# Kernel tuning notes

Hardware: AMD Instinct MI355X
Metric: run time of the kernel (lower is better)

Reference implementation:

```python
import jax, jax.numpy as jnp
import numpy as np

D_K = 64


def setup_inputs() -> dict:
    key = jax.random.key(0)
    ks = jax.random.split(key, 12)
    b, n, t, k = 16, 2048, 12, 32
    d_q, d_k, d_c, n_head, d_out = 32, 64, 10, 4, 32
    return {
        "x": jax.random.normal(ks[0], (b, n, t, k), dtype=jnp.float32),
        "dis_mat": jax.random.uniform(ks[1], (n, n), dtype=jnp.float32),
        "K_S": jax.random.normal(ks[2], (n_head, d_k), dtype=jnp.float32) * 0.1,
        "V_S": jax.random.normal(ks[3], (n_head, n, d_c), dtype=jnp.float32) * 0.05,
        "K_T": jax.random.normal(ks[4], (n_head, d_k), dtype=jnp.float32) * 0.1,
        "V_T": jax.random.normal(ks[5], (n_head, n, d_c), dtype=jnp.float32) * 0.05,
        "W_Q0": jax.random.normal(ks[6], (k, d_q), dtype=jnp.float32) * 0.1,
        "W_QS": jax.random.normal(ks[7], (n * d_q, d_k), dtype=jnp.float32) * 0.01,
        "W_QT": jax.random.normal(ks[8], (t * d_q, d_k), dtype=jnp.float32) * 0.05,
        "W2": jax.random.normal(ks[9], (k, d_out), dtype=jnp.float32) * 0.1,
        "W_s0": jax.random.normal(ks[10], (k, d_out), dtype=jnp.float32) * 0.1,
        "W_s1": jax.random.normal(ks[11], (k, d_out), dtype=jnp.float32) * 0.1,
    }


def reference(x, dis_mat, K_S, V_S, K_T, V_T, W_Q0, W_QS, W_QT, W2, W_s0, W_s1):
    b, n, t, k = x.shape
    scale = 1.0 / jnp.sqrt(jnp.float32(D_K))
    # Q_0 projection: [b,n,t,d_q]
    out = x @ W_Q0
    # temporal / spatial queries -> [b, d_k]
    qt = out.mean(axis=1).reshape(b, -1) @ W_QT
    qs = out.mean(axis=2).reshape(b, -1) @ W_QS
    # head attention weights: [b, n_head]
    attn_t = jax.nn.softmax((qt * scale) @ K_T.T, axis=1)
    attn_s = jax.nn.softmax((qs * scale) @ K_S.T, axis=1)
    # head-mixed node embeddings: [b, n, d_c]
    et = jnp.einsum('hnc,bh->bnc', V_T, attn_t)
    es = jnp.einsum('hnc,bh->bnc', V_S, attn_s)
    ets = et + es
    # dynamic adjacency: [b, n, n]
    adj = jnp.einsum('bnc,bmc->bnm', ets, ets)
    adj = jax.nn.softmax(jax.nn.relu(dis_mat[None] + adj), axis=2)
    # graph conv chain over [b, t, n, d_out]
    xp = jnp.transpose(x, (0, 2, 1, 3))  # [b,t,n,k]
    z = xp @ W2
    for W in (W_s0, W_s1):
        z = jnp.einsum('bnm,btmd->btnd', adj, z) + xp @ W
    return jnp.transpose(z, (0, 2, 1, 3))  # [b,n,t,d_out]
```

## Files before the change

kernel.cpp:

```cpp
#include <hip/hip_runtime.h>

typedef __bf16 bf16x8 __attribute__((ext_vector_type(8)));
typedef float f32x4 __attribute__((ext_vector_type(4)));

__device__ __forceinline__ unsigned short f2bf(float f) {
  unsigned u = __builtin_bit_cast(unsigned, f);
  u += 0x7fffu + ((u >> 16) & 1u);
  return (unsigned short)(u >> 16);
}
__device__ __forceinline__ float bf2f(unsigned short h) {
  unsigned u = ((unsigned)h) << 16;
  return __builtin_bit_cast(float, u);
}
__device__ __forceinline__ void gload16(const void* g, void* l) {
  __builtin_amdgcn_global_load_lds((const __attribute__((address_space(1))) void*)g,
                                   (__attribute__((address_space(3))) void*)l, 16, 0, 0);
}
__device__ __forceinline__ int perm7(int x) {
  return ((x >> 3) & 3) * 32 + ((x >> 5) << 3) + (x & 7);
}


__global__ __launch_bounds__(256) void k_qs(const float* __restrict__ x,
                                            const float* __restrict__ W_Q0,
                                            const float* __restrict__ W_QS,
                                            float* __restrict__ pqs) {
  __shared__ __align__(16) float w0[1024];
  __shared__ __align__(16) float lm[1024];
  __shared__ float lq[1024];
  __shared__ float red[4][16][64];
  const int tid = threadIdx.x;
#pragma unroll
  for (int i = 0; i < 4; ++i) w0[tid + i * 256] = W_Q0[tid + i * 256];
  const int n0 = blockIdx.x * 2;

  {
    const int b = tid >> 4, r = tid & 15, n = r >> 3, k4 = r & 7;
    const float4* xp = (const float4*)(x + ((size_t)(b * 2048 + n0 + n) * 12) * 32) + k4;
    float4 s0 = xp[0], s1 = xp[8], s2 = xp[16];
    float4 s3 = xp[24], s4 = xp[32], s5 = xp[40];
#pragma unroll
    for (int t = 6; t < 12; ++t) {
      float4 v = xp[t * 8];
      s0.x += v.x; s0.y += v.y; s0.z += v.z; s0.w += v.w;
      float4 tmp = s0; s0 = s1; s1 = s2; s2 = s3; s3 = s4; s4 = s5; s5 = tmp;
    }
    float4 m;
    m.x = (s0.x + s1.x + s2.x) + (s3.x + s4.x + s5.x);
    m.y = (s0.y + s1.y + s2.y) + (s3.y + s4.y + s5.y);
    m.z = (s0.z + s1.z + s2.z) + (s3.z + s4.z + s5.z);
    m.w = (s0.w + s1.w + s2.w) + (s3.w + s4.w + s5.w);
    const float inv12 = 1.0f / 12.0f;
    m.x *= inv12; m.y *= inv12; m.z *= inv12; m.w *= inv12;
    *(float4*)(lm + (b * 2 + n) * 32 + k4 * 4) = m;
  }
  __syncthreads();
#pragma unroll
  for (int j = 0; j < 4; ++j) {
    int i = tid + j * 256;
    int bn = i >> 5, q = i & 31;
    const float* mrow = &lm[bn * 32];
    float a = 0.f;
#pragma unroll
    for (int k = 0; k < 32; ++k) a += mrow[k] * w0[k * 32 + q];
    lq[i] = a;
  }
  __syncthreads();
  const int lane = tid & 63, w = tid >> 6;
  float acc[16];
#pragma unroll
  for (int b = 0; b < 16; ++b) acc[b] = 0.f;
#pragma unroll
  for (int rl = 0; rl < 16; ++rl) {
    int r = w * 16 + rl;
    float wv = W_QS[(size_t)(n0 * 32 + r) * 64 + lane];
#pragma unroll
    for (int b = 0; b < 16; ++b) acc[b] += lq[b * 64 + r] * wv;
  }
#pragma unroll
  for (int b = 0; b < 16; ++b) red[w][b][lane] = acc[b];
  __syncthreads();
#pragma unroll
  for (int it = 0; it < 4; ++it) {
    int idx = tid + it * 256;
    float s = red[0][idx >> 6][idx & 63] + red[1][idx >> 6][idx & 63] +
              red[2][idx >> 6][idx & 63] + red[3][idx >> 6][idx & 63];
    pqs[(size_t)blockIdx.x * 1024 + idx] = s;
  }
}

__global__ __launch_bounds__(256) void k_head(const float* __restrict__ pqs,
                                              const float* __restrict__ pxmn_p,
                                              const float* __restrict__ W_Q0,
                                              const float* __restrict__ W_QT,
                                              const float* __restrict__ K_T,
                                              const float* __restrict__ K_S,
                                              float* __restrict__ at_g) {
  const int b = blockIdx.x, tid = threadIdx.x;
  __shared__ float red[4][64];
  __shared__ float qs_s[64];
  __shared__ float xmn_s[384];
  __shared__ float xp[384];
  __shared__ float qtp[4][64];

  {
    const int q = tid >> 6, dk = tid & 63;
    const float* p = pqs + (size_t)(q * 256) * 1024 + b * 64 + dk;
    float s0 = 0.f, s1 = 0.f, s2 = 0.f, s3 = 0.f;
#pragma unroll
    for (int c = 0; c < 256; c += 4) {
      s0 += p[(size_t)(c + 0) * 1024];
      s1 += p[(size_t)(c + 1) * 1024];
      s2 += p[(size_t)(c + 2) * 1024];
      s3 += p[(size_t)(c + 3) * 1024];
    }
    red[q][dk] = (s0 + s1) + (s2 + s3);
  }
  for (int i = tid; i < 384; i += 256) {
    int t = i >> 5, k = i & 31;
    const float* p = pxmn_p + (size_t)((b * 12 + t) * 8) * 32 + k;
    float v = ((p[0] + p[32]) + (p[64] + p[96])) + ((p[128] + p[160]) + (p[192] + p[224]));
    xmn_s[i] = v * (1.0f / 2048.0f);
  }
  __syncthreads();
  for (int i = tid; i < 384; i += 256) {
    int t = i >> 5, q = i & 31;
    float a = 0.f;
#pragma unroll
    for (int k = 0; k < 32; ++k) a += xmn_s[t * 32 + k] * W_Q0[k * 32 + q];
    xp[i] = a;
  }
  if (tid < 64) qs_s[tid] = red[0][tid] + red[1][tid] + red[2][tid] + red[3][tid];
  __syncthreads();
  {
    const int w = tid >> 6, dk = tid & 63;
    const float* wq = W_QT + (size_t)(w * 96) * 64 + dk;
    const float* xw = xp + w * 96;
    float a0 = 0.f, a1 = 0.f, a2 = 0.f;
#pragma unroll
    for (int i = 0; i < 96; i += 3) {
      a0 += xw[i + 0] * wq[(size_t)(i + 0) * 64];
      a1 += xw[i + 1] * wq[(size_t)(i + 1) * 64];
      a2 += xw[i + 2] * wq[(size_t)(i + 2) * 64];
    }
    qtp[w][dk] = (a0 + a1) + a2;
  }
  __syncthreads();
  if (tid < 64) {
    int lane = tid;
    float qtv = qtp[0][lane] + qtp[1][lane] + qtp[2][lane] + qtp[3][lane];
    float qsv = qs_s[lane];
    float lt[4], ls[4];
#pragma unroll
    for (int h = 0; h < 4; ++h) {
      float p = qtv * K_T[h * 64 + lane];
#pragma unroll
      for (int off = 32; off > 0; off >>= 1) p += __shfl_xor(p, off);
      lt[h] = p;
      float p2 = qsv * K_S[h * 64 + lane];
#pragma unroll
      for (int off = 32; off > 0; off >>= 1) p2 += __shfl_xor(p2, off);
      ls[h] = p2;
    }
    if (lane == 0) {
      const float scale = 0.125f;
      float mt = fmaxf(fmaxf(lt[0], lt[1]), fmaxf(lt[2], lt[3]));
      float ms = fmaxf(fmaxf(ls[0], ls[1]), fmaxf(ls[2], ls[3]));
      float et[4], es[4], st = 0.f, ss = 0.f;
#pragma unroll
      for (int h = 0; h < 4; ++h) {
        et[h] = __expf((lt[h] - mt) * scale); st += et[h];
        es[h] = __expf((ls[h] - ms) * scale); ss += es[h];
      }
#pragma unroll
      for (int h = 0; h < 4; ++h) {
        at_g[b * 8 + h] = et[h] / st;
        at_g[b * 8 + 4 + h] = es[h] / ss;
      }
    }
  }
}

__global__ __launch_bounds__(256) void k_ets(const float* __restrict__ at_g,
                                             const float* __restrict__ V_T,
                                             const float* __restrict__ V_S,
                                             unsigned short* __restrict__ ets_bf) {
  int idx = blockIdx.x * 256 + threadIdx.x;
  int b = idx >> 11, n = idx & 2047;
  const float* at = at_g + b * 8;
  float a0 = at[0], a1 = at[1], a2 = at[2], a3 = at[3];
  float s0 = at[4], s1 = at[5], s2 = at[6], s3 = at[7];
  float v[10];
#pragma unroll
  for (int c = 0; c < 10; ++c) {
    int o = n * 10 + c;
    v[c] = a0 * V_T[o] + a1 * V_T[20480 + o] + a2 * V_T[40960 + o] + a3 * V_T[61440 + o] +
           s0 * V_S[o] + s1 * V_S[20480 + o] + s2 * V_S[40960 + o] + s3 * V_S[61440 + o];
  }
  uint4 lo, hi;
  lo.x = (unsigned)f2bf(v[0]) | ((unsigned)f2bf(v[1]) << 16);
  lo.y = (unsigned)f2bf(v[2]) | ((unsigned)f2bf(v[3]) << 16);
  lo.z = (unsigned)f2bf(v[4]) | ((unsigned)f2bf(v[5]) << 16);
  lo.w = (unsigned)f2bf(v[6]) | ((unsigned)f2bf(v[7]) << 16);
  hi.x = (unsigned)f2bf(v[8]) | ((unsigned)f2bf(v[9]) << 16);
  hi.y = 0; hi.z = 0; hi.w = 0;
  *(uint4*)(ets_bf + (size_t)idx * 16) = lo;
  *(uint4*)(ets_bf + (size_t)idx * 16 + 8) = hi;
}


__global__ __launch_bounds__(512, 4) void k_adj(const unsigned short* __restrict__ ets_bf,
                                                const float* __restrict__ dis,
                                                unsigned char* __restrict__ adjf) {
  __shared__ __align__(16) unsigned char Tws[8 * 4352];
  __shared__ float st_sum[8][16];
  __shared__ float rowinv_s[16];

  const int tid = threadIdx.x;
  const int lane = tid & 63;
  const int w = tid >> 6;
  const int cl = lane & 15;
  const int g = lane >> 4;
  const int orig = blockIdx.x;
  const int work = (orig & 7) * 256 + (orig >> 3);
  const int b = work & 15;
  const int n0 = (work >> 4) << 4;

  const unsigned char* gets = (const unsigned char*)(ets_bf + (size_t)b * 32768);

  uint4 araw = *(const uint4*)(ets_bf + ((size_t)b * 2048 + n0 + cl) * 16 + (g & 1) * 8);
  if (g >= 2) { araw.x = 0; araw.y = 0; araw.z = 0; araw.w = 0; }
  bf16x8 strip = __builtin_bit_cast(bf16x8, araw);

  f32x4 acc[16];
  const int cbase = (w << 8) + cl;
#pragma unroll
  for (int n = 0; n < 16; ++n) {
    uint4 braw = *(const uint4*)(gets + (size_t)(cbase + n * 16) * 32 + (g & 1) * 16);
    if (g >= 2) { braw.x = 0; braw.y = 0; braw.z = 0; braw.w = 0; }
    bf16x8 nodes = __builtin_bit_cast(bf16x8, braw);
    acc[n] = __builtin_amdgcn_mfma_f32_16x16x32_bf16(nodes, strip,
                                                     (f32x4){0.f, 0.f, 0.f, 0.f}, 0, 0, 0);
  }

  const float* drow = dis + (size_t)(n0 + cl) * 2048 + (w << 8) + (g << 2);
  float lsum = 0.f;
#pragma unroll
  for (int n = 0; n < 16; ++n) {
    float4 dv = *(const float4*)(drow + n * 16);
    float e0 = __expf(fmaxf(acc[n][0] + dv.x, 0.f));
    float e1 = __expf(fmaxf(acc[n][1] + dv.y, 0.f));
    float e2 = __expf(fmaxf(acc[n][2] + dv.z, 0.f));
    float e3 = __expf(fmaxf(acc[n][3] + dv.w, 0.f));
    acc[n][0] = e0; acc[n][1] = e1; acc[n][2] = e2; acc[n][3] = e3;
    lsum += (e0 + e1) + (e2 + e3);
  }
  lsum += __shfl_xor(lsum, 16);
  lsum += __shfl_xor(lsum, 32);
  if (g == 0) st_sum[w][cl] = lsum;
  __syncthreads();
  if (tid < 16) {
    float s = st_sum[0][tid];
#pragma unroll
    for (int ww = 1; ww < 8; ++ww) s += st_sum[ww][tid];
    rowinv_s[tid] = 256.0f / s;
  }
  __syncthreads();

  const float inv = rowinv_s[cl];
  unsigned char* Tw = Tws + w * 4352;
#pragma unroll
  for (int n = 0; n < 16; ++n) {
    int ml = n * 16 + (g << 2);
    int pb = ((ml >> 7) << 7) + perm7(ml & 127);
    unsigned u = __builtin_amdgcn_cvt_pk_fp8_f32(acc[n][0] * inv, acc[n][1] * inv, 0, false);
    u = __builtin_amdgcn_cvt_pk_fp8_f32(acc[n][2] * inv, acc[n][3] * inv, (int)u, true);
    *(unsigned*)(Tw + cl * 272 + pb) = u;
  }
  asm volatile("s_waitcnt lgkmcnt(0)" ::: "memory");

  unsigned char* obase = adjf + ((size_t)(b * 2048 + n0)) * 2048 + (w << 8);
  const int rw = lane >> 4;
  const int cc = (lane & 15) * 16;
#pragma unroll
  for (int q = 0; q < 4; ++q) {
    int row = q * 4 + rw;
    uint4 v = *(const uint4*)(Tw + row * 272 + cc);
    *(uint4*)(obase + (size_t)row * 2048 + cc) = v;
  }
}


__global__ __launch_bounds__(256) void k_zb(const float* __restrict__ x,
                                            const float* __restrict__ W2,
                                            const float* __restrict__ Ws0,
                                            const float* __restrict__ Ws1,
                                            unsigned char* __restrict__ z0Tf,
                                            unsigned short* __restrict__ bias0T,
                                            unsigned short* __restrict__ bias1T,
                                            float* __restrict__ pxmn_p) {
  __shared__ __align__(16) unsigned short wlds[3072];
  __shared__ __align__(16) unsigned char zsh[32 * 272];
  __shared__ __align__(16) unsigned char b0sh[32 * 528];
  __shared__ __align__(16) unsigned char b1sh[32 * 528];
  __shared__ float psum[4][32];
  const int tid = threadIdx.x;
  for (int j = tid; j < 3072; j += 256) {
    int mat = j >> 10, rr = j & 1023, k = rr >> 5, d = rr & 31;
    const float* Wsrc = (mat == 0) ? W2 : (mat == 1 ? Ws0 : Ws1);
    wlds[(mat * 32 + d) * 32 + k] = f2bf(Wsrc[rr]);
  }
  __syncthreads();

  const int lane = tid & 63, w = tid >> 6;
  const int cl = lane & 15, g = lane >> 4;
  const int bx = blockIdx.x;
  const int b = bx / 96, r = bx % 96, t = r >> 3, mc = r & 7;

  bf16x8 bfr[6];
#pragma unroll
  for (int dt = 0; dt < 6; ++dt)
    bfr[dt] = *(const bf16x8*)(wlds + (dt * 16 + cl) * 32 + g * 8);

  const float* gx = x + ((size_t)(b * 2048 + mc * 256 + w * 64 + cl) * 12 + t) * 32 + g * 8;

  float4 sx0 = {0.f, 0.f, 0.f, 0.f}, sx1 = {0.f, 0.f, 0.f, 0.f};
#pragma unroll
  for (int i = 0; i < 4; ++i) {
    const float* xp = gx + (size_t)i * 16 * 384;
    float4 v0 = *(const float4*)xp;
    float4 v1 = *(const float4*)(xp + 4);
    sx0.x += v0.x; sx0.y += v0.y; sx0.z += v0.z; sx0.w += v0.w;
    sx1.x += v1.x; sx1.y += v1.y; sx1.z += v1.z; sx1.w += v1.w;
    bf16x8 af;
    af[0] = (__bf16)v0.x; af[1] = (__bf16)v0.y; af[2] = (__bf16)v0.z; af[3] = (__bf16)v0.w;
    af[4] = (__bf16)v1.x; af[5] = (__bf16)v1.y; af[6] = (__bf16)v1.z; af[7] = (__bf16)v1.w;
    f32x4 acc[6];
#pragma unroll
    for (int dt = 0; dt < 6; ++dt)
      acc[dt] = __builtin_amdgcn_mfma_f32_16x16x32_bf16(af, bfr[dt],
                                                        (f32x4){0.f, 0.f, 0.f, 0.f}, 0, 0, 0);
    const int ml = w * 64 + i * 16 + g * 4;
    const int pb = ((ml >> 7) << 7) + perm7(ml & 127);
#pragma unroll
    for (int dt = 0; dt < 2; ++dt) {
      unsigned u = __builtin_amdgcn_cvt_pk_fp8_f32(acc[dt][0], acc[dt][1], 0, false);
      u = __builtin_amdgcn_cvt_pk_fp8_f32(acc[dt][2], acc[dt][3], (int)u, true);
      *(unsigned*)(zsh + (dt * 16 + cl) * 272 + pb) = u;
    }
#pragma unroll
    for (int dt = 0; dt < 2; ++dt) {
      uint2 p;
      p.x = (unsigned)f2bf(acc[2 + dt][0]) | ((unsigned)f2bf(acc[2 + dt][1]) << 16);
      p.y = (unsigned)f2bf(acc[2 + dt][2]) | ((unsigned)f2bf(acc[2 + dt][3]) << 16);
      *(uint2*)(b0sh + (dt * 16 + cl) * 528 + ml * 2) = p;
      uint2 q;
      q.x = (unsigned)f2bf(acc[4 + dt][0]) | ((unsigned)f2bf(acc[4 + dt][1]) << 16);
      q.y = (unsigned)f2bf(acc[4 + dt][2]) | ((unsigned)f2bf(acc[4 + dt][3]) << 16);
      *(uint2*)(b1sh + (dt * 16 + cl) * 528 + ml * 2) = q;
    }
  }
#pragma unroll
  for (int off = 1; off < 16; off <<= 1) {
    sx0.x += __shfl_xor(sx0.x, off); sx0.y += __shfl_xor(sx0.y, off);
    sx0.z += __shfl_xor(sx0.z, off); sx0.w += __shfl_xor(sx0.w, off);
    sx1.x += __shfl_xor(sx1.x, off); sx1.y += __shfl_xor(sx1.y, off);
    sx1.z += __shfl_xor(sx1.z, off); sx1.w += __shfl_xor(sx1.w, off);
  }
  if (cl == 0) {
    *(float4*)(&psum[w][g * 8]) = sx0;
    *(float4*)(&psum[w][g * 8 + 4]) = sx1;
  }
  __syncthreads();
  if (tid < 32)
    pxmn_p[(size_t)((b * 12 + t) * 8 + mc) * 32 + tid] =
        psum[0][tid] + psum[1][tid] + psum[2][tid] + psum[3][tid];

  const int d = tid >> 3, c8 = tid & 7;
  {
    uint4 v0 = *(const uint4*)(zsh + d * 272 + c8 * 32);
    uint4 v1 = *(const uint4*)(zsh + d * 272 + c8 * 32 + 16);
    unsigned char* zdst =
        z0Tf + (size_t)b * 786432 + (size_t)(t * 32 + d) * 2048 + mc * 256 + c8 * 32;
    *(uint4*)zdst = v0;
    *(uint4*)(zdst + 16) = v1;
  }
  {
    char* bdst0 = (char*)(bias0T + (size_t)b * 786432 + (size_t)(t * 32 + d) * 2048 +
                          mc * 256 + c8 * 32);
    char* bdst1 = (char*)(bias1T + (size_t)b * 786432 + (size_t)(t * 32 + d) * 2048 +
                          mc * 256 + c8 * 32);
#pragma unroll
    for (int q = 0; q < 4; ++q) {
      *(uint4*)(bdst0 + q * 16) = *(const uint4*)(b0sh + d * 528 + c8 * 64 + q * 16);
      *(uint4*)(bdst1 + q * 16) = *(const uint4*)(b1sh + d * 528 + c8 * 64 + q * 16);
    }
  }
}


template <int OUT_F32>
__global__ __launch_bounds__(256, 2) void gemm_adj(const unsigned char* __restrict__ adjf,
                                                   const unsigned char* __restrict__ Bt,
                                                   const unsigned short* __restrict__ biasT,
                                                   void* __restrict__ outp) {
  const int tid = threadIdx.x;
  const int lane = tid & 63;
  const int wid = tid >> 6;
  const int wr = wid >> 1, wc = wid & 1;
  const int orig = blockIdx.x;
  const int wg = (orig & 7) * 64 + (orig >> 3);
  const int b = wg >> 5;
  const int w32 = wg & 31;
  const int m0 = ((w32 >> 1) & 15) << 7;
  const int c0 = (w32 & 1) * 192;

  __shared__ __align__(16) unsigned char smem[81920];

  const unsigned char* aBase = adjf + ((size_t)b << 22);
  const unsigned char* bBase = Bt + (size_t)b * 786432;
  const int jx = ((tid & 7) ^ ((tid >> 3) & 7)) << 4;
  const unsigned char* gA = aBase + (size_t)(m0 + (tid >> 3)) * 2048 + jx;
  const unsigned char* gB = bBase + (size_t)(c0 + (tid >> 3)) * 2048 + jx;

  int aoff[2][4], boff[2][6];
#pragma unroll
  for (int kkp = 0; kkp < 2; ++kkp) {
    int c = ((lane >> 4) << 1) + kkp;
#pragma unroll
    for (int f = 0; f < 4; ++f) {
      int rA = wr * 64 + f * 16 + (lane & 15);
      aoff[kkp][f] = rA * 128 + ((c ^ (rA & 7)) << 4);
    }
#pragma unroll
    for (int n = 0; n < 6; ++n) {
      int rB = wc * 96 + n * 16 + (lane & 15);
      boff[kkp][n] = 16384 + rB * 128 + ((c ^ (rB & 7)) << 4);
    }
  }

  f32x4 acc[4][6] = {};

#define STAGE(BUF, KT)                                                               \
  {                                                                                  \
    _Pragma("unroll") for (int ii = 0; ii < 4; ++ii)                                 \
        gload16(gA + (size_t)ii * 65536 + (KT)*128, smem + (BUF) + ii * 4096 + tid * 16); \
    _Pragma("unroll") for (int ii = 0; ii < 6; ++ii)                                 \
        gload16(gB + (size_t)ii * 65536 + (KT)*128,                                  \
                smem + (BUF) + 16384 + ii * 4096 + tid * 16);                        \
  }

  STAGE(0, 0);

  int cur = 0;
  for (int kt = 0; kt < 16; ++kt) {
    const int nxt = cur ^ 40960;
    if (kt < 15) {
      STAGE(nxt, kt + 1);
      asm volatile("s_waitcnt vmcnt(10)" ::: "memory");
    } else {
      asm volatile("s_waitcnt vmcnt(0)" ::: "memory");
    }
    __builtin_amdgcn_s_barrier();
#pragma unroll
    for (int kkp = 0; kkp < 2; ++kkp) {
      ulong2 av[4], bv[6];
#pragma unroll
      for (int f = 0; f < 4; ++f) av[f] = *(const ulong2*)(smem + cur + aoff[kkp][f]);
#pragma unroll
      for (int n = 0; n < 6; ++n) bv[n] = *(const ulong2*)(smem + cur + boff[kkp][n]);
#pragma unroll
      for (int m = 0; m < 4; ++m)
#pragma unroll
        for (int n = 0; n < 6; ++n)
          acc[m][n] = __builtin_amdgcn_mfma_f32_16x16x32_fp8_fp8(
              (long)av[m].x, (long)bv[n].x, acc[m][n], 0, 0, 0);
#pragma unroll
      for (int m = 0; m < 4; ++m)
#pragma unroll
        for (int n = 0; n < 6; ++n)
          acc[m][n] = __builtin_amdgcn_mfma_f32_16x16x32_fp8_fp8(
              (long)av[m].y, (long)bv[n].y, acc[m][n], 0, 0, 0);
    }
    __builtin_amdgcn_s_barrier();
    cur = nxt;
  }
#undef STAGE

  const float inv256 = 0.00390625f;
  const int cl = lane & 15;
  const int r4 = (lane >> 4) << 2;
  const unsigned short* bi = biasT + (size_t)b * 786432;
  if (OUT_F32) {
    float* o = (float*)outp + (size_t)b * 786432;
#pragma unroll
    for (int m = 0; m < 4; ++m) {
      int row0 = m0 + wr * 64 + m * 16 + r4;
#pragma unroll
      for (int n = 0; n < 6; ++n) {
        int col = c0 + wc * 96 + n * 16 + cl;
        uint2 bw = *(const uint2*)(bi + ((size_t)col << 11) + row0);
        float bv0 = bf2f((unsigned short)(bw.x & 0xffff));
        float bv1 = bf2f((unsigned short)(bw.x >> 16));
        float bv2 = bf2f((unsigned short)(bw.y & 0xffff));
        float bv3 = bf2f((unsigned short)(bw.y >> 16));
        o[(size_t)(row0 + 0) * 384 + col] = acc[m][n][0] * inv256 + bv0;
        o[(size_t)(row0 + 1) * 384 + col] = acc[m][n][1] * inv256 + bv1;
        o[(size_t)(row0 + 2) * 384 + col] = acc[m][n][2] * inv256 + bv2;
        o[(size_t)(row0 + 3) * 384 + col] = acc[m][n][3] * inv256 + bv3;
      }
    }
  } else {
    unsigned char* o = (unsigned char*)outp + (size_t)b * 786432;
#pragma unroll
    for (int m = 0; m < 4; ++m) {
      int row0 = m0 + wr * 64 + m * 16 + r4;
      const int pb = ((row0 >> 7) << 7) + perm7(row0 & 127);
#pragma unroll
      for (int n = 0; n < 6; ++n) {
        int col = c0 + wc * 96 + n * 16 + cl;
        uint2 bw = *(const uint2*)(bi + ((size_t)col << 11) + row0);
        float v0 = acc[m][n][0] * inv256 + bf2f((unsigned short)(bw.x & 0xffff));
        float v1 = acc[m][n][1] * inv256 + bf2f((unsigned short)(bw.x >> 16));
        float v2 = acc[m][n][2] * inv256 + bf2f((unsigned short)(bw.y & 0xffff));
        float v3 = acc[m][n][3] * inv256 + bf2f((unsigned short)(bw.y >> 16));
        unsigned u = __builtin_amdgcn_cvt_pk_fp8_f32(v0, v1, 0, false);
        u = __builtin_amdgcn_cvt_pk_fp8_f32(v2, v3, (int)u, true);
        *(unsigned*)(o + (size_t)col * 2048 + pb) = u;
      }
    }
  }
}


extern "C" void kernel_launch(void* const* d_in, const int* in_sizes, int n_in,
                              void* d_out, int out_size, void* d_ws, size_t ws_size,
                              hipStream_t stream) {
  const float* x = (const float*)d_in[0];
  const float* dis = (const float*)d_in[1];
  const float* K_S = (const float*)d_in[2];
  const float* V_S = (const float*)d_in[3];
  const float* K_T = (const float*)d_in[4];
  const float* V_T = (const float*)d_in[5];
  const float* W_Q0 = (const float*)d_in[6];
  const float* W_QS = (const float*)d_in[7];
  const float* W_QT = (const float*)d_in[8];
  const float* W2 = (const float*)d_in[9];
  const float* W_s0 = (const float*)d_in[10];
  const float* W_s1 = (const float*)d_in[11];

  char* ws = (char*)d_ws;
  float* pxmn_p = (float*)(ws + 0);
  float* pqs = (float*)(ws + 196608);
  unsigned short* ets_bf = (unsigned short*)(ws + 4390912);
  unsigned char* adjf = (unsigned char*)(ws + 5439488);
  unsigned char* z0Tf = (unsigned char*)(ws + 72548352);
  unsigned char* z1Tf = (unsigned char*)(ws + 85131264);
  unsigned short* bias0T = (unsigned short*)(ws + 97714176);
  unsigned short* bias1T = (unsigned short*)(ws + 122880000);
  float* at_g = (float*)(ws + 148045824);

  k_qs<<<1024, 256, 0, stream>>>(x, W_Q0, W_QS, pqs);
  k_zb<<<1536, 256, 0, stream>>>(x, W2, W_s0, W_s1, z0Tf, bias0T, bias1T, pxmn_p);
  k_head<<<16, 256, 0, stream>>>(pqs, pxmn_p, W_Q0, W_QT, K_T, K_S, at_g);
  k_ets<<<128, 256, 0, stream>>>(at_g, V_T, V_S, ets_bf);
  k_adj<<<2048, 512, 0, stream>>>(ets_bf, dis, adjf);
  gemm_adj<0><<<512, 256, 0, stream>>>(adjf, z0Tf, bias0T, (void*)z1Tf);
  gemm_adj<1><<<512, 256, 0, stream>>>(adjf, z1Tf, bias1T, d_out);
}
```

Before: 194.9 us.

## Fuse adjacency softmax construction into both graph-conv GEMMs, drop adj buffer

Removes the separate k_adj kernel and its 64MB fp8 adjacency buffer. Each GEMM block now recomputes its own 128-row adjacency tile per K-step: a bf16 MFMA of ets against ets, plus the dis_mat add, relu, exp and fp8 pack written into LDS. Softmax normalisation is deferred to the epilogue using rowsums accumulated during the loop. This trades the adjacency write and the two re-reads for recomputing the scores twice and re-reading dis_mat (fp32, 16MB) in each GEMM. It also risks fp8 precision, since unnormalized exp values are quantized instead of values scaled by 256/sum.

```diff
diff --git a/kernel.cpp b/kernel.cpp
--- a/kernel.cpp
+++ b/kernel.cpp
@@ -206,88 +206,6 @@
   hi.y = 0; hi.z = 0; hi.w = 0;
   *(uint4*)(ets_bf + (size_t)idx * 16) = lo;
   *(uint4*)(ets_bf + (size_t)idx * 16 + 8) = hi;
-}
-
-
-__global__ __launch_bounds__(512, 4) void k_adj(const unsigned short* __restrict__ ets_bf,
-                                                const float* __restrict__ dis,
-                                                unsigned char* __restrict__ adjf) {
-  __shared__ __align__(16) unsigned char Tws[8 * 4352];
-  __shared__ float st_sum[8][16];
-  __shared__ float rowinv_s[16];
-
-  const int tid = threadIdx.x;
-  const int lane = tid & 63;
-  const int w = tid >> 6;
-  const int cl = lane & 15;
-  const int g = lane >> 4;
-  const int orig = blockIdx.x;
-  const int work = (orig & 7) * 256 + (orig >> 3);
-  const int b = work & 15;
-  const int n0 = (work >> 4) << 4;
-
-  const unsigned char* gets = (const unsigned char*)(ets_bf + (size_t)b * 32768);
-
-  uint4 araw = *(const uint4*)(ets_bf + ((size_t)b * 2048 + n0 + cl) * 16 + (g & 1) * 8);
-  if (g >= 2) { araw.x = 0; araw.y = 0; araw.z = 0; araw.w = 0; }
-  bf16x8 strip = __builtin_bit_cast(bf16x8, araw);
-
-  f32x4 acc[16];
-  const int cbase = (w << 8) + cl;
-#pragma unroll
-  for (int n = 0; n < 16; ++n) {
-    uint4 braw = *(const uint4*)(gets + (size_t)(cbase + n * 16) * 32 + (g & 1) * 16);
-    if (g >= 2) { braw.x = 0; braw.y = 0; braw.z = 0; braw.w = 0; }
-    bf16x8 nodes = __builtin_bit_cast(bf16x8, braw);
-    acc[n] = __builtin_amdgcn_mfma_f32_16x16x32_bf16(nodes, strip,
-                                                     (f32x4){0.f, 0.f, 0.f, 0.f}, 0, 0, 0);
-  }
-
-  const float* drow = dis + (size_t)(n0 + cl) * 2048 + (w << 8) + (g << 2);
-  float lsum = 0.f;
-#pragma unroll
-  for (int n = 0; n < 16; ++n) {
-    float4 dv = *(const float4*)(drow + n * 16);
-    float e0 = __expf(fmaxf(acc[n][0] + dv.x, 0.f));
-    float e1 = __expf(fmaxf(acc[n][1] + dv.y, 0.f));
-    float e2 = __expf(fmaxf(acc[n][2] + dv.z, 0.f));
-    float e3 = __expf(fmaxf(acc[n][3] + dv.w, 0.f));
-    acc[n][0] = e0; acc[n][1] = e1; acc[n][2] = e2; acc[n][3] = e3;
-    lsum += (e0 + e1) + (e2 + e3);
-  }
-  lsum += __shfl_xor(lsum, 16);
-  lsum += __shfl_xor(lsum, 32);
-  if (g == 0) st_sum[w][cl] = lsum;
-  __syncthreads();
-  if (tid < 16) {
-    float s = st_sum[0][tid];
-#pragma unroll
-    for (int ww = 1; ww < 8; ++ww) s += st_sum[ww][tid];
-    rowinv_s[tid] = 256.0f / s;
-  }
-  __syncthreads();
-
-  const float inv = rowinv_s[cl];
-  unsigned char* Tw = Tws + w * 4352;
-#pragma unroll
-  for (int n = 0; n < 16; ++n) {
-    int ml = n * 16 + (g << 2);
-    int pb = ((ml >> 7) << 7) + perm7(ml & 127);
-    unsigned u = __builtin_amdgcn_cvt_pk_fp8_f32(acc[n][0] * inv, acc[n][1] * inv, 0, false);
-    u = __builtin_amdgcn_cvt_pk_fp8_f32(acc[n][2] * inv, acc[n][3] * inv, (int)u, true);
-    *(unsigned*)(Tw + cl * 272 + pb) = u;
-  }
-  asm volatile("s_waitcnt lgkmcnt(0)" ::: "memory");
-
-  unsigned char* obase = adjf + ((size_t)(b * 2048 + n0)) * 2048 + (w << 8);
-  const int rw = lane >> 4;
-  const int cc = (lane & 15) * 16;
-#pragma unroll
-  for (int q = 0; q < 4; ++q) {
-    int row = q * 4 + rw;
-    uint4 v = *(const uint4*)(Tw + row * 272 + cc);
-    *(uint4*)(obase + (size_t)row * 2048 + cc) = v;
-  }
 }
 
 
@@ -400,14 +318,17 @@
 
 
 template <int OUT_F32>
-__global__ __launch_bounds__(256, 2) void gemm_adj(const unsigned char* __restrict__ adjf,
-                                                   const unsigned char* __restrict__ Bt,
-                                                   const unsigned short* __restrict__ biasT,
-                                                   void* __restrict__ outp) {
+__global__ __launch_bounds__(256, 2) void gemm_fused(const unsigned short* __restrict__ ets_bf,
+                                                     const float* __restrict__ dis,
+                                                     const unsigned char* __restrict__ Bt,
+                                                     const unsigned short* __restrict__ biasT,
+                                                     void* __restrict__ outp) {
   const int tid = threadIdx.x;
   const int lane = tid & 63;
-  const int wid = tid >> 6;
-  const int wr = wid >> 1, wc = wid & 1;
+  const int w = tid >> 6;
+  const int cl = lane & 15;
+  const int g = lane >> 4;
+  const int wr = w >> 1, wc = w & 1;
   const int orig = blockIdx.x;
   const int wg = (orig & 7) * 64 + (orig >> 3);
   const int b = wg >> 5;
@@ -415,13 +336,22 @@
   const int m0 = ((w32 >> 1) & 15) << 7;
   const int c0 = (w32 & 1) * 192;
 
-  __shared__ __align__(16) unsigned char smem[81920];
-
-  const unsigned char* aBase = adjf + ((size_t)b << 22);
+  __shared__ __align__(16) unsigned char smem[16384 + 49152];
+  __shared__ float rs_lds[128];
+
+  const unsigned char* gets = (const unsigned char*)(ets_bf + (size_t)b * 32768);
   const unsigned char* bBase = Bt + (size_t)b * 786432;
   const int jx = ((tid & 7) ^ ((tid >> 3) & 7)) << 4;
-  const unsigned char* gA = aBase + (size_t)(m0 + (tid >> 3)) * 2048 + jx;
   const unsigned char* gB = bBase + (size_t)(c0 + (tid >> 3)) * 2048 + jx;
+
+  bf16x8 strip[2];
+#pragma unroll
+  for (int s = 0; s < 2; ++s) {
+    uint4 a = *(const uint4*)(ets_bf + ((size_t)b * 2048 + m0 + (2 * w + s) * 16 + cl) * 16 +
+                              (g & 1) * 8);
+    if (g >= 2) { a.x = 0; a.y = 0; a.z = 0; a.w = 0; }
+    strip[s] = __builtin_bit_cast(bf16x8, a);
+  }
 
   int aoff[2][4], boff[2][6];
 #pragma unroll
@@ -435,40 +365,77 @@
 #pragma unroll
     for (int n = 0; n < 6; ++n) {
       int rB = wc * 96 + n * 16 + (lane & 15);
-      boff[kkp][n] = 16384 + rB * 128 + ((c ^ (rB & 7)) << 4);
+      boff[kkp][n] = rB * 128 + ((c ^ (rB & 7)) << 4);
     }
   }
 
   f32x4 acc[4][6] = {};
-
-#define STAGE(BUF, KT)                                                               \
-  {                                                                                  \
-    _Pragma("unroll") for (int ii = 0; ii < 4; ++ii)                                 \
-        gload16(gA + (size_t)ii * 65536 + (KT)*128, smem + (BUF) + ii * 4096 + tid * 16); \
-    _Pragma("unroll") for (int ii = 0; ii < 6; ++ii)                                 \
-        gload16(gB + (size_t)ii * 65536 + (KT)*128,                                  \
-                smem + (BUF) + 16384 + ii * 4096 + tid * 16);                        \
-  }
-
-  STAGE(0, 0);
+  float rowsum[2] = {0.f, 0.f};
+
+#define STAGEZ(BUF, KT)                                                            \
+  {                                                                                \
+    _Pragma("unroll") for (int ii = 0; ii < 6; ++ii)                               \
+        gload16(gB + (size_t)ii * 65536 + (KT)*128,                                \
+                smem + 16384 + (BUF) + ii * 4096 + tid * 16);                      \
+  }
+
+  STAGEZ(0, 0);
 
   int cur = 0;
   for (int kt = 0; kt < 16; ++kt) {
-    const int nxt = cur ^ 40960;
+    const int nxt = cur ^ 24576;
+    if (kt < 15) STAGEZ(nxt, kt + 1);
+
+    uint4 nraw[8];
+#pragma unroll
+    for (int n = 0; n < 8; ++n) {
+      uint4 r = *(const uint4*)(gets + (size_t)(kt * 128 + n * 16 + cl) * 32 + (g & 1) * 16);
+      if (g >= 2) { r.x = 0; r.y = 0; r.z = 0; r.w = 0; }
+      nraw[n] = r;
+    }
+#pragma unroll
+    for (int s = 0; s < 2; ++s) {
+      const int rA = (2 * w + s) * 16 + cl;
+      const float* drow = dis + (size_t)(m0 + rA) * 2048 + kt * 128 + (g << 2);
+      f32x4 sc[8];
+#pragma unroll
+      for (int n = 0; n < 8; ++n)
+        sc[n] = __builtin_amdgcn_mfma_f32_16x16x32_bf16(__builtin_bit_cast(bf16x8, nraw[n]),
+                                                        strip[s], (f32x4){0.f, 0.f, 0.f, 0.f},
+                                                        0, 0, 0);
+      const int sw = (rA & 7) << 4;
+#pragma unroll
+      for (int n = 0; n < 8; ++n) {
+        float4 dv = *(const float4*)(drow + n * 16);
+        float e0 = __expf(fmaxf(sc[n][0] + dv.x, 0.f));
+        float e1 = __expf(fmaxf(sc[n][1] + dv.y, 0.f));
+        float e2 = __expf(fmaxf(sc[n][2] + dv.z, 0.f));
+        float e3 = __expf(fmaxf(sc[n][3] + dv.w, 0.f));
+        rowsum[s] += (e0 + e1) + (e2 + e3);
+        int ml = n * 16 + (g << 2);
+        int pb = perm7(ml);
+        int byte = rA * 128 + (((pb & 0xF0) ^ sw) | (pb & 15));
+        unsigned u = __builtin_amdgcn_cvt_pk_fp8_f32(e0, e1, 0, false);
+        u = __builtin_amdgcn_cvt_pk_fp8_f32(e2, e3, (int)u, true);
+        *(unsigned*)(smem + byte) = u;
+      }
+    }
+    asm volatile("s_waitcnt lgkmcnt(0)" ::: "memory");
     if (kt < 15) {
-      STAGE(nxt, kt + 1);
-      asm volatile("s_waitcnt vmcnt(10)" ::: "memory");
+      asm volatile("s_waitcnt vmcnt(6)" ::: "memory");
     } else {
       asm volatile("s_waitcnt vmcnt(0)" ::: "memory");
     }
     __builtin_amdgcn_s_barrier();
+
 #pragma unroll
     for (int kkp = 0; kkp < 2; ++kkp) {
       ulong2 av[4], bv[6];
 #pragma unroll
-      for (int f = 0; f < 4; ++f) av[f] = *(const ulong2*)(smem + cur + aoff[kkp][f]);
-#pragma unroll
-      for (int n = 0; n < 6; ++n) bv[n] = *(const ulong2*)(smem + cur + boff[kkp][n]);
+      for (int f = 0; f < 4; ++f) av[f] = *(const ulong2*)(smem + aoff[kkp][f]);
+#pragma unroll
+      for (int n = 0; n < 6; ++n)
+        bv[n] = *(const ulong2*)(smem + 16384 + cur + boff[kkp][n]);
 #pragma unroll
       for (int m = 0; m < 4; ++m)
 #pragma unroll
@@ -483,47 +450,63 @@
               (long)av[m].y, (long)bv[n].y, acc[m][n], 0, 0, 0);
     }
     __builtin_amdgcn_s_barrier();
+    asm volatile("" ::: "memory");
     cur = nxt;
   }
-#undef STAGE
-
-  const float inv256 = 0.00390625f;
-  const int cl = lane & 15;
+#undef STAGEZ
+
+  rowsum[0] += __shfl_xor(rowsum[0], 16);
+  rowsum[0] += __shfl_xor(rowsum[0], 32);
+  rowsum[1] += __shfl_xor(rowsum[1], 16);
+  rowsum[1] += __shfl_xor(rowsum[1], 32);
+  if (lane < 16) {
+    rs_lds[(2 * w + 0) * 16 + cl] = rowsum[0];
+    rs_lds[(2 * w + 1) * 16 + cl] = rowsum[1];
+  }
+  __syncthreads();
+
+  const int epcl = lane & 15;
   const int r4 = (lane >> 4) << 2;
   const unsigned short* bi = biasT + (size_t)b * 786432;
   if (OUT_F32) {
     float* o = (float*)outp + (size_t)b * 786432;
 #pragma unroll
     for (int m = 0; m < 4; ++m) {
-      int row0 = m0 + wr * 64 + m * 16 + r4;
+      int rloc = wr * 64 + m * 16 + r4;
+      int row0 = m0 + rloc;
+      float4 rsv = *(const float4*)(rs_lds + rloc);
+      float i0 = 1.0f / rsv.x, i1 = 1.0f / rsv.y, i2 = 1.0f / rsv.z, i3 = 1.0f / rsv.w;
 #pragma unroll
       for (int n = 0; n < 6; ++n) {
-        int col = c0 + wc * 96 + n * 16 + cl;
+        int col = c0 + wc * 96 + n * 16 + epcl;
         uint2 bw = *(const uint2*)(bi + ((size_t)col << 11) + row0);
-        float bv0 = bf2f((unsigned short)(bw.x & 0xffff));
-        float bv1 = bf2f((unsigned short)(bw.x >> 16));
-        float bv2 = bf2f((unsigned short)(bw.y & 0xffff));
-        float bv3 = bf2f((unsigned short)(bw.y >> 16));
-        o[(size_t)(row0 + 0) * 384 + col] = acc[m][n][0] * inv256 + bv0;
-        o[(size_t)(row0 + 1) * 384 + col] = acc[m][n][1] * inv256 + bv1;
-        o[(size_t)(row0 + 2) * 384 + col] = acc[m][n][2] * inv256 + bv2;
-        o[(size_t)(row0 + 3) * 384 + col] = acc[m][n][3] * inv256 + bv3;
+        o[(size_t)(row0 + 0) * 384 + col] =
+            acc[m][n][0] * i0 + bf2f((unsigned short)(bw.x & 0xffff));
+        o[(size_t)(row0 + 1) * 384 + col] =
+            acc[m][n][1] * i1 + bf2f((unsigned short)(bw.x >> 16));
+        o[(size_t)(row0 + 2) * 384 + col] =
+            acc[m][n][2] * i2 + bf2f((unsigned short)(bw.y & 0xffff));
+        o[(size_t)(row0 + 3) * 384 + col] =
+            acc[m][n][3] * i3 + bf2f((unsigned short)(bw.y >> 16));
       }
     }
   } else {
     unsigned char* o = (unsigned char*)outp + (size_t)b * 786432;
 #pragma unroll
     for (int m = 0; m < 4; ++m) {
-      int row0 = m0 + wr * 64 + m * 16 + r4;
+      int rloc = wr * 64 + m * 16 + r4;
+      int row0 = m0 + rloc;
+      float4 rsv = *(const float4*)(rs_lds + rloc);
+      float i0 = 1.0f / rsv.x, i1 = 1.0f / rsv.y, i2 = 1.0f / rsv.z, i3 = 1.0f / rsv.w;
       const int pb = ((row0 >> 7) << 7) + perm7(row0 & 127);
 #pragma unroll
       for (int n = 0; n < 6; ++n) {
-        int col = c0 + wc * 96 + n * 16 + cl;
+        int col = c0 + wc * 96 + n * 16 + epcl;
         uint2 bw = *(const uint2*)(bi + ((size_t)col << 11) + row0);
-        float v0 = acc[m][n][0] * inv256 + bf2f((unsigned short)(bw.x & 0xffff));
-        float v1 = acc[m][n][1] * inv256 + bf2f((unsigned short)(bw.x >> 16));
-        float v2 = acc[m][n][2] * inv256 + bf2f((unsigned short)(bw.y & 0xffff));
-        float v3 = acc[m][n][3] * inv256 + bf2f((unsigned short)(bw.y >> 16));
+        float v0 = acc[m][n][0] * i0 + bf2f((unsigned short)(bw.x & 0xffff));
+        float v1 = acc[m][n][1] * i1 + bf2f((unsigned short)(bw.x >> 16));
+        float v2 = acc[m][n][2] * i2 + bf2f((unsigned short)(bw.y & 0xffff));
+        float v3 = acc[m][n][3] * i3 + bf2f((unsigned short)(bw.y >> 16));
         unsigned u = __builtin_amdgcn_cvt_pk_fp8_f32(v0, v1, 0, false);
         u = __builtin_amdgcn_cvt_pk_fp8_f32(v2, v3, (int)u, true);
         *(unsigned*)(o + (size_t)col * 2048 + pb) = u;
@@ -553,18 +536,16 @@
   float* pxmn_p = (float*)(ws + 0);
   float* pqs = (float*)(ws + 196608);
   unsigned short* ets_bf = (unsigned short*)(ws + 4390912);
-  unsigned char* adjf = (unsigned char*)(ws + 5439488);
-  unsigned char* z0Tf = (unsigned char*)(ws + 72548352);
-  unsigned char* z1Tf = (unsigned char*)(ws + 85131264);
-  unsigned short* bias0T = (unsigned short*)(ws + 97714176);
-  unsigned short* bias1T = (unsigned short*)(ws + 122880000);
-  float* at_g = (float*)(ws + 148045824);
+  unsigned char* z0Tf = (unsigned char*)(ws + 5439488);
+  unsigned char* z1Tf = (unsigned char*)(ws + 18022400);
+  unsigned short* bias0T = (unsigned short*)(ws + 30605312);
+  unsigned short* bias1T = (unsigned short*)(ws + 55771136);
+  float* at_g = (float*)(ws + 80936960);
 
   k_qs<<<1024, 256, 0, stream>>>(x, W_Q0, W_QS, pqs);
   k_zb<<<1536, 256, 0, stream>>>(x, W2, W_s0, W_s1, z0Tf, bias0T, bias1T, pxmn_p);
   k_head<<<16, 256, 0, stream>>>(pqs, pxmn_p, W_Q0, W_QT, K_T, K_S, at_g);
   k_ets<<<128, 256, 0, stream>>>(at_g, V_T, V_S, ets_bf);
-  k_adj<<<2048, 512, 0, stream>>>(ets_bf, dis, adjf);
-  gemm_adj<0><<<512, 256, 0, stream>>>(adjf, z0Tf, bias0T, (void*)z1Tf);
-  gemm_adj<1><<<512, 256, 0, stream>>>(adjf, z1Tf, bias1T, d_out);
-}
+  gemm_fused<0><<<512, 256, 0, stream>>>(ets_bf, dis, z0Tf, bias0T, (void*)z1Tf);
+  gemm_fused<1><<<512, 256, 0, stream>>>(ets_bf, dis, z1Tf, bias1T, d_out);
+}
```

Result: slower. 273.1 us (+40.1%).
